# Performance work log

Measured on AMD Instinct MI355X. Metric: run time of the kernel, lower is better.

## Reference

```python
import jax, jax.numpy as jnp
import numpy as np

B, L, S, D = 32, 256, 4, 512
H = L * S  # history_capacity
TGB = 128
VOCAB = 50000
LN_EPS = 1e-5


def _layer_norm(x, gamma, beta):
    mu = jnp.mean(x, axis=-1, keepdims=True)
    var = jnp.var(x, axis=-1, keepdims=True)
    return (x - mu) * jax.lax.rsqrt(var + LN_EPS) * gamma + beta


def setup_inputs() -> dict:
    key = jax.random.key(0)
    ks = jax.random.split(key, 16)
    inp = {
        'embed_table': jax.random.normal(ks[0], (VOCAB, D), jnp.float32) * 0.02,
        'time_gap_emb': jax.random.normal(ks[1], (TGB + 1, D), jnp.float32) * 0.02,
        'seq_id_emb': jax.random.normal(ks[2], (S + 1, D), jnp.float32) * 0.02,
        'pos_emb': jax.random.normal(ks[3], (L, D), jnp.float32) * 0.02,
        'ln_gamma': jnp.ones((5 * D,), jnp.float32),
        'ln_beta': jnp.zeros((5 * D,), jnp.float32),
        'w1': jax.random.normal(ks[4], (5 * D, 4 * D), jnp.float32) * (1.0 / np.sqrt(5 * D)),
        'b1': jnp.zeros((4 * D,), jnp.float32),
        'w2': jax.random.normal(ks[5], (4 * D, D), jnp.float32) * (1.0 / np.sqrt(4 * D)),
        'b2': jnp.zeros((D,), jnp.float32),
        'empty_tokens': jax.random.normal(ks[6], (S, D), jnp.float32) * 0.02,
        'history_tokens': jax.random.randint(ks[7], (B, H), 0, VOCAB, jnp.int64 if jax.config.jax_enable_x64 else jnp.int32),
        'post_tokens': jax.random.randint(ks[8], (B, H), 0, VOCAB),
        'author_tokens': jax.random.randint(ks[9], (B, H), 0, VOCAB),
        'action_tokens': jax.random.randint(ks[10], (B, H), 0, VOCAB),
        'time_gap': jax.random.randint(ks[11], (B, H), 0, TGB + 1),
        'group_ids': jax.random.randint(ks[12], (B, H), 0, S + 1),
        'lengths': jax.random.randint(ks[13], (B,), 0, H + 1),
    }
    return inp


def reference(embed_table, time_gap_emb, seq_id_emb, pos_emb, ln_gamma, ln_beta,
              w1, b1, w2, b2, empty_tokens,
              history_tokens, post_tokens, author_tokens, action_tokens,
              time_gap, group_ids, lengths):
    # padded-dense validity mask: positions < lengths  [B,H]
    history_mask = jnp.arange(H)[None, :] < lengths[:, None]
    # zero out padded tokens (to_padded_dense pads with 0)
    hm_i = history_mask.astype(history_tokens.dtype)
    ht = history_tokens * hm_i
    pt = post_tokens * hm_i
    at = author_tokens * hm_i
    ct = action_tokens * hm_i
    tg = jnp.clip(time_gap * hm_i, 0, TGB)
    gid = group_ids * hm_i

    # event feature: 4 token embeds + time-gap embed -> [B,H,5D]
    event_inputs = jnp.concatenate(
        [embed_table[ht], embed_table[pt], embed_table[at], embed_table[ct],
         time_gap_emb[tg]], axis=-1)
    x = _layer_norm(event_inputs, ln_gamma, ln_beta)
    h = jax.nn.silu(x @ w1 + b1)          # dropout is eval-mode no-op
    event_tokens = h @ w2 + b2            # [B,H,D]

    # per-(batch, group) bucketization: keep last L valid positions of each group
    grp = jnp.arange(1, S + 1)
    mask_bs = history_mask[:, None, :] & (gid[:, None, :] == grp[None, :, None])  # [B,S,H]
    cum = jnp.cumsum(mask_bs.astype(jnp.int32), axis=-1)
    count = cum[..., -1]                                  # [B,S]
    offset = jnp.maximum(count - L, 0)                    # drop all but last L
    rank0 = cum - 1
    keep = mask_bs & (rank0 >= offset[..., None])
    dest = jnp.where(keep, rank0 - offset[..., None], L)  # slot L = dump slot

    def scatter_one(tokens, d):  # tokens [H,D], d [H] -> [L,D]
        return jnp.zeros((L + 1, D), tokens.dtype).at[d].set(tokens)[:L]

    # vmap over batch then group
    states = jax.vmap(lambda tok, ds: jax.vmap(lambda d: scatter_one(tok, d))(ds))(
        event_tokens, dest)                               # [B,S,L,D]

    # empty groups get the learned empty token at slot 0
    is_empty = (count == 0)                               # [B,S]
    slot0 = (jnp.arange(L) == 0)                          # [L]
    states = jnp.where((is_empty[:, :, None] & slot0[None, None, :])[..., None],
                       empty_tokens[None, :, None, :], states)
    kept = jnp.where(is_empty, 1, jnp.minimum(count, L))  # [B,S]
    sequence_mask = jnp.arange(L)[None, None, :] < kept[..., None]  # [B,S,L]

    states = states + pos_emb[None, None, :, :] + seq_id_emb[1:][None, :, None, :]
    states = states * sequence_mask[..., None].astype(states.dtype)
    return states, sequence_mask
```

## Files before the change

### kernel.cpp

```cpp
#include <hip/hip_runtime.h>
#include <hip/hip_bf16.h>
#include <stdint.h>

#define NB 32
#define NL 256
#define NS 4
#define ND 512
#define NH 1024
#define FIVE_D 2560
#define HID 2048
#define MMAX 32768

typedef __bf16 bf16_t;
typedef __bf16 bf16x4 __attribute__((ext_vector_type(4)));
typedef __bf16 bf16x8 __attribute__((ext_vector_type(8)));
typedef float f32x4 __attribute__((ext_vector_type(4)));

__device__ __forceinline__ void async_ld16(const void* g, void* l) {
  __builtin_amdgcn_global_load_lds(
      (__attribute__((address_space(1))) void*)(uintptr_t)g,
      (__attribute__((address_space(3))) void*)(uintptr_t)l, 16, 0, 0);
}

__global__ void build_index_kernel(const int* __restrict__ group_ids,
                                   const int* __restrict__ lengths,
                                   int* __restrict__ n_rows,
                                   int* __restrict__ row_src,
                                   int* __restrict__ row_dst,
                                   const float* __restrict__ empty_tokens,
                                   const float* __restrict__ pos_emb,
                                   const float* __restrict__ seq_emb,
                                   float* __restrict__ out,
                                   float* __restrict__ mask) {
  const int g = blockIdx.x >> 2;
  const int qtr = blockIdx.x & 3;
  const int b = g >> 2, s = g & 3;
  const int t = threadIdx.x;
  const int lane = t & 63, w = t >> 6;
  int len = lengths[b];
  len = len < 0 ? 0 : (len > NH ? NH : len);
  const int* gi = group_ids + b * NH;

  __shared__ int wtot[16];
  __shared__ int sbase;

  bool valid[4];
#pragma unroll
  for (int c = 0; c < 4; ++c) {
    int h = c * 256 + t;
    valid[c] = (h < len) && (gi[h] == s + 1);
    unsigned long long m = __ballot(valid[c]);
    if (lane == 0) wtot[c * 4 + w] = __popcll(m);
  }
  __syncthreads();

  int pre[16];
  int run = 0;
#pragma unroll
  for (int i = 0; i < 16; ++i) { pre[i] = run; run += wtot[i]; }
  const int count = run;
  const int keff = count < NL ? count : NL;
  const int offset = count - keff;

  const bool empty = (count == 0);
  const int start = empty ? 1 : keff;

  if (qtr == 0) {
    if (t == 0) sbase = atomicAdd(n_rows, keff);
    __syncthreads();
    const int base = sbase;

    const unsigned long long lt = (1ull << lane) - 1ull;
#pragma unroll
    for (int c = 0; c < 4; ++c) {
      unsigned long long m = __ballot(valid[c]);
      if (valid[c]) {
        int rank = pre[c * 4 + w] + __popcll(m & lt);
        if (rank >= offset) {
          int slot = rank - offset;
          row_src[base + slot] = b * NH + c * 256 + t;
          row_dst[base + slot] = g * NL + slot;
        }
      }
    }

    const int keptm = empty ? 1 : keff;
    mask[g * NL + t] = (t < keptm) ? 1.f : 0.f;

    if (empty) {
      float* basep = out + (size_t)g * NL * ND;
      for (int d = t; d < ND; d += 256)
        basep[d] = empty_tokens[s * ND + d] + pos_emb[d] +
                   seq_emb[(s + 1) * ND + d];
    }
  }

  int lo = qtr * 64; if (lo < start) lo = start;
  const int hi = qtr * 64 + 64;
  if (lo < hi) {
    uint4* p = (uint4*)(out + (size_t)g * NL * ND);
    uint4 z; z.x = z.y = z.z = z.w = 0u;
    for (int i = lo * (ND / 4) + t; i < hi * (ND / 4); i += 256) p[i] = z;
  }
}

template <int KD, int NDIM>
__global__ void transpose_cvt_kernel(const float* __restrict__ src,
                                     bf16_t* __restrict__ dst) {
  __shared__ float tile[32][33];
  int k0 = blockIdx.y * 32, n0 = blockIdx.x * 32;
  int tx = threadIdx.x & 31, ty = threadIdx.x >> 5;
#pragma unroll
  for (int i = 0; i < 32; i += 8)
    tile[ty + i][tx] = src[(size_t)(k0 + ty + i) * NDIM + n0 + tx];
  __syncthreads();
#pragma unroll
  for (int i = 0; i < 32; i += 8)
    dst[(size_t)(n0 + ty + i) * KD + k0 + tx] = (bf16_t)tile[tx][ty + i];
}

__launch_bounds__(256)
__global__ void gather_ln_kernel(const float* __restrict__ embed,
                                 const float* __restrict__ tg_emb,
                                 const int* __restrict__ ht,
                                 const int* __restrict__ pt,
                                 const int* __restrict__ at,
                                 const int* __restrict__ ct,
                                 const int* __restrict__ tg,
                                 const float* __restrict__ gamma,
                                 const float* __restrict__ beta,
                                 const int* __restrict__ n_rows,
                                 const int* __restrict__ row_src,
                                 int row_base, int chunk,
                                 bf16_t* __restrict__ X) {
  const int l = threadIdx.x & 63;
  const int wid = blockIdx.x * 4 + (threadIdx.x >> 6);
  const int wstride = gridDim.x * 4;
  const int M = *n_rows;
  int lim = row_base + chunk;
  if (lim > M) lim = M;

  const int o = l * 4;

  for (int r = row_base + wid; r < lim; r += wstride) {
    const int rl = r - row_base;
    const int pos = row_src[r];

    const float* s0 = embed + (size_t)ht[pos] * ND;
    const float* s1 = embed + (size_t)pt[pos] * ND;
    const float* s2 = embed + (size_t)at[pos] * ND;
    const float* s3 = embed + (size_t)ct[pos] * ND;
    int tgv = tg[pos];
    tgv = tgv < 0 ? 0 : (tgv > 128 ? 128 : tgv);
    const float* s4 = tg_emb + (size_t)tgv * ND;

    float4 v0 = *(const float4*)(s0 + o);
    float4 v1 = *(const float4*)(s0 + 256 + o);
    float4 v2 = *(const float4*)(s1 + o);
    float4 v3 = *(const float4*)(s1 + 256 + o);
    float4 v4 = *(const float4*)(s2 + o);
    float4 v5 = *(const float4*)(s2 + 256 + o);
    float4 v6 = *(const float4*)(s3 + o);
    float4 v7 = *(const float4*)(s3 + 256 + o);
    float4 v8 = *(const float4*)(s4 + o);
    float4 v9 = *(const float4*)(s4 + 256 + o);

    float sum = 0.f, sq = 0.f;
#define ACC(vk)                                                              \
    do {                                                                     \
      sum += vk.x + vk.y + vk.z + vk.w;                                      \
      sq += vk.x * vk.x + vk.y * vk.y + vk.z * vk.z + vk.w * vk.w;           \
    } while (0)
    ACC(v0); ACC(v1); ACC(v2); ACC(v3); ACC(v4);
    ACC(v5); ACC(v6); ACC(v7); ACC(v8); ACC(v9);
#undef ACC
#pragma unroll
    for (int off = 32; off > 0; off >>= 1) {
      sum += __shfl_xor(sum, off);
      sq += __shfl_xor(sq, off);
    }
    const float mu = sum * (1.f / FIVE_D);
    const float var = sq * (1.f / FIVE_D) - mu * mu;
    const float rstd = rsqrtf(var + 1e-5f);

    bf16_t* xr = X + (size_t)rl * FIVE_D;
#define LN_STORE(vk, kofs)                                                   \
    do {                                                                     \
      float4 gm = *(const float4*)(gamma + (kofs) + o);                      \
      float4 bt = *(const float4*)(beta + (kofs) + o);                       \
      bf16x4 ov;                                                             \
      ov[0] = (bf16_t)((vk.x - mu) * rstd * gm.x + bt.x);                    \
      ov[1] = (bf16_t)((vk.y - mu) * rstd * gm.y + bt.y);                    \
      ov[2] = (bf16_t)((vk.z - mu) * rstd * gm.z + bt.z);                    \
      ov[3] = (bf16_t)((vk.w - mu) * rstd * gm.w + bt.w);                    \
      *(bf16x4*)(xr + (kofs) + o) = ov;                                      \
    } while (0)
    LN_STORE(v0, 0);    LN_STORE(v1, 256);
    LN_STORE(v2, 512);  LN_STORE(v3, 768);
    LN_STORE(v4, 1024); LN_STORE(v5, 1280);
    LN_STORE(v6, 1536); LN_STORE(v7, 1792);
    LN_STORE(v8, 2048); LN_STORE(v9, 2304);
#undef LN_STORE
  }
}

#define FENCE asm volatile("" ::: "memory")
#define BARRIER do { FENCE; __builtin_amdgcn_s_barrier(); FENCE; } while (0)
#define WAIT_VM(n) asm volatile("s_waitcnt vmcnt(" #n ")" ::: "memory")

template <int KD, int LDC>
__launch_bounds__(512, 2)
__global__ void gemm256p4_kernel(const bf16_t* __restrict__ A,
                                 const bf16_t* __restrict__ Bt,
                                 const int* __restrict__ nrows_p,
                                 int row_base,
                                 const float* __restrict__ bias,
                                 bf16_t* __restrict__ Cb) {
  static_assert(KD % 64 == 0 && KD / 64 >= 2, "KD");
  const int M = *nrows_p;
  const int m0 = blockIdx.x * 256;
  if (row_base + m0 >= M) return;
  const int n0 = blockIdx.y * 256;

  extern __shared__ char smem[];

  const int t = threadIdx.x;
  const int lane = t & 63;
  const int wv = t >> 6;
  const int wm = wv >> 2;
  const int wn = wv & 3;
  const int l15 = lane & 15;
  const int l4 = lane >> 4;

  const int r0 = t >> 3;
  const int sq = (t & 7) ^ (r0 & 7);
  const bf16_t* Ab = A + (size_t)(m0 + r0) * KD + sq * 8;
  const bf16_t* Bb =
      Bt + (size_t)(n0 + (r0 >> 5) * 64 + (r0 & 31)) * KD + sq * 8;
  const int dst16 = t * 16;

  const int cs0 = (l4 ^ (l15 & 7)) << 4;
  const int cs1 = cs0 ^ 64;
  const int arow = (wm * 64 + l15) * 128;
  const int brow = (wn * 32 + l15) * 128;

  f32x4 acc[2][2][4][2] = {};
  bf16x8 a[4][2], bl[2][2], bh[2][2];

#define SA(dbuf, h, kofs)                                                    \
  do {                                                                       \
    char* _d = smem + (dbuf) * 65536 + (h) * 16384 + dst16;                  \
    async_ld16(Ab + (size_t)((h) * 64) * KD + (kofs), _d);                   \
    async_ld16(Ab + (size_t)((h) * 64 + 128) * KD + (kofs), _d + 8192);      \
  } while (0)
#define SB(dbuf, h, kofs)                                                    \
  do {                                                                       \
    char* _d = smem + (dbuf) * 65536 + 32768 + (h) * 16384 + dst16;          \
    async_ld16(Bb + (size_t)((h) * 32) * KD + (kofs), _d);                   \
    async_ld16(Bb + (size_t)((h) * 32 + 128) * KD + (kofs), _d + 8192);      \
  } while (0)
#define LA(cbuf, ih)                                                         \
  do {                                                                       \
    const char* _s = smem + (cbuf) * 65536 + (ih) * 16384 + arow;            \
    _Pragma("unroll") for (int _i = 0; _i < 4; ++_i) {                       \
      a[_i][0] = *(const bf16x8*)(_s + _i * 2048 + cs0);                     \
      a[_i][1] = *(const bf16x8*)(_s + _i * 2048 + cs1);                     \
    }                                                                        \
  } while (0)
#define LB(dst, cbuf, jh)                                                    \
  do {                                                                       \
    const char* _s = smem + (cbuf) * 65536 + 32768 + (jh) * 16384 + brow;    \
    _Pragma("unroll") for (int _j = 0; _j < 2; ++_j) {                       \
      dst[_j][0] = *(const bf16x8*)(_s + _j * 2048 + cs0);                   \
      dst[_j][1] = *(const bf16x8*)(_s + _j * 2048 + cs1);                   \
    }                                                                        \
  } while (0)
#define MMA(ih, jh, B)                                                       \
  do {                                                                       \
    _Pragma("unroll") for (int _i = 0; _i < 4; ++_i)                         \
    _Pragma("unroll") for (int _j = 0; _j < 2; ++_j) {                       \
      acc[ih][jh][_i][_j] = __builtin_amdgcn_mfma_f32_16x16x32_bf16(         \
          a[_i][0], B[_j][0], acc[ih][jh][_i][_j], 0, 0, 0);                 \
      acc[ih][jh][_i][_j] = __builtin_amdgcn_mfma_f32_16x16x32_bf16(         \
          a[_i][1], B[_j][1], acc[ih][jh][_i][_j], 0, 0, 0);                 \
    }                                                                        \
  } while (0)

  constexpr int NT = KD / 64;

  SA(0, 0, 0);
  SB(0, 0, 0);
  SB(0, 1, 0);
  SA(0, 1, 0);

  int c = 0;
  for (int tk = 1; tk < NT; ++tk) {
    const int kn = tk * 64;
    const int d = c ^ 1;
    WAIT_VM(4);
    BARRIER;
    LA(c, 0);
    LB(bl, c, 0);
    SA(d, 0, kn);
    __builtin_amdgcn_s_setprio(1);
    MMA(0, 0, bl);
    __builtin_amdgcn_s_setprio(0);
    WAIT_VM(4);
    BARRIER;
    LB(bh, c, 1);
    SB(d, 0, kn);
    __builtin_amdgcn_s_setprio(1);
    MMA(0, 1, bh);
    __builtin_amdgcn_s_setprio(0);
    WAIT_VM(4);
    BARRIER;
    LA(c, 1);
    SB(d, 1, kn);
    __builtin_amdgcn_s_setprio(1);
    MMA(1, 1, bh);
    __builtin_amdgcn_s_setprio(0);
    SA(d, 1, kn);
    __builtin_amdgcn_s_setprio(1);
    MMA(1, 0, bl);
    __builtin_amdgcn_s_setprio(0);
    BARRIER;
    c = d;
  }

  WAIT_VM(4);
  BARRIER;
  LA(c, 0);
  LB(bl, c, 0);
  MMA(0, 0, bl);
  WAIT_VM(2);
  BARRIER;
  LB(bh, c, 1);
  MMA(0, 1, bh);
  WAIT_VM(0);
  BARRIER;
  LA(c, 1);
  MMA(1, 1, bh);
  MMA(1, 0, bl);

#pragma unroll
  for (int ih = 0; ih < 2; ++ih)
#pragma unroll
    for (int i = 0; i < 4; ++i) {
      const int rbase = m0 + wm * 128 + ih * 64 + i * 16 + l4 * 4;
#pragma unroll
      for (int jh = 0; jh < 2; ++jh)
#pragma unroll
        for (int j = 0; j < 2; ++j) {
          const int n = n0 + wn * 64 + jh * 32 + j * 16 + l15;
          const float bn = bias[n];
#pragma unroll
          for (int q = 0; q < 4; ++q) {
            float v = acc[ih][jh][i][j][q] + bn;
            v = v / (1.f + __expf(-v));
            Cb[(size_t)(rbase + q) * LDC + n] = (bf16_t)v;
          }
        }
    }
#undef SA
#undef SB
#undef LA
#undef LB
#undef MMA
}

template <int KD>
__launch_bounds__(512, 4)
__global__ void gemm128_scatter_kernel(const bf16_t* __restrict__ A,
                                       const bf16_t* __restrict__ Bt,
                                       const int* __restrict__ nrows_p,
                                       int row_base,
                                       const float* __restrict__ bias,
                                       const int* __restrict__ row_dst,
                                       const float* __restrict__ pos_emb,
                                       const float* __restrict__ seq_emb,
                                       float* __restrict__ out) {
  static_assert(KD % 64 == 0 && KD / 64 >= 2, "KD");
  const int M = *nrows_p;
  const int m0 = blockIdx.x * 128;
  if (row_base + m0 >= M) return;
  const int n0 = blockIdx.y * 128;

  extern __shared__ char smem[];

  const int t = threadIdx.x;
  const int lane = t & 63;
  const int wv = t >> 6;
  const int wm = wv >> 1;
  const int wn = wv & 1;
  const int l15 = lane & 15;
  const int l4 = lane >> 4;

  const int r0 = t >> 3;
  const int sq = (t & 7) ^ (r0 & 7);
  const bf16_t* Ab = A + (size_t)(m0 + r0) * KD + sq * 8;
  const bf16_t* Bb = Bt + (size_t)(n0 + r0) * KD + sq * 8;
  const int dst16 = t * 16;

  const int cs0 = (l4 ^ (l15 & 7)) << 4;
  const int cs1 = cs0 ^ 64;
  const int arow = (wm * 32 + l15) * 128;
  const int brow = (wn * 64 + l15) * 128;

  f32x4 acc[2][4] = {};
  bf16x8 a[2][2], b[4][2];

#define STAGE_A2(dbuf, kofs)                                                 \
  do {                                                                       \
    char* _d = smem + (dbuf) * 32768 + dst16;                                \
    async_ld16(Ab + (kofs), _d);                                             \
    async_ld16(Ab + (size_t)64 * KD + (kofs), _d + 8192);                    \
  } while (0)
#define STAGE_B2(dbuf, kofs)                                                 \
  do {                                                                       \
    char* _d = smem + (dbuf) * 32768 + 16384 + dst16;                        \
    async_ld16(Bb + (kofs), _d);                                             \
    async_ld16(Bb + (size_t)64 * KD + (kofs), _d + 8192);                    \
  } while (0)
#define LOAD_A2(cbuf)                                                        \
  do {                                                                       \
    const char* _s = smem + (cbuf) * 32768 + arow;                           \
    _Pragma("unroll") for (int _i = 0; _i < 2; ++_i) {                       \
      a[_i][0] = *(const bf16x8*)(_s + _i * 2048 + cs0);                     \
      a[_i][1] = *(const bf16x8*)(_s + _i * 2048 + cs1);                     \
    }                                                                        \
  } while (0)
#define LOAD_B2(cbuf)                                                        \
  do {                                                                       \
    const char* _s = smem + (cbuf) * 32768 + 16384 + brow;                   \
    _Pragma("unroll") for (int _j = 0; _j < 4; ++_j) {                       \
      b[_j][0] = *(const bf16x8*)(_s + _j * 2048 + cs0);                     \
      b[_j][1] = *(const bf16x8*)(_s + _j * 2048 + cs1);                     \
    }                                                                        \
  } while (0)
#define MMA2                                                                 \
  do {                                                                       \
    _Pragma("unroll") for (int _i = 0; _i < 2; ++_i)                         \
    _Pragma("unroll") for (int _j = 0; _j < 4; ++_j) {                       \
      acc[_i][_j] = __builtin_amdgcn_mfma_f32_16x16x32_bf16(                 \
          a[_i][0], b[_j][0], acc[_i][_j], 0, 0, 0);                         \
      acc[_i][_j] = __builtin_amdgcn_mfma_f32_16x16x32_bf16(                 \
          a[_i][1], b[_j][1], acc[_i][_j], 0, 0, 0);                         \
    }                                                                        \
  } while (0)

  constexpr int NT = KD / 64;

  STAGE_A2(0, 0);
  STAGE_B2(0, 0);

  int c = 0;
  for (int tk = 1; tk < NT; ++tk) {
    const int kn = tk * 64;
    const int d = c ^ 1;
    STAGE_A2(d, kn);
    WAIT_VM(2);
    BARRIER;
    LOAD_A2(c);
    LOAD_B2(c);
    STAGE_B2(d, kn);
    __builtin_amdgcn_s_setprio(1);
    MMA2;
    __builtin_amdgcn_s_setprio(0);
    BARRIER;
    c = d;
  }

  WAIT_VM(0);
  BARRIER;
  LOAD_A2(c);
  LOAD_B2(c);
  MMA2;

#pragma unroll
  for (int i = 0; i < 2; ++i) {
    int mbase = m0 + wm * 32 + i * 16 + l4 * 4;
#pragma unroll
    for (int q = 0; q < 4; ++q) {
      int r = mbase + q;
      if (row_base + r >= M) continue;
      int dst = row_dst[row_base + r];
      int slot = dst & (NL - 1);
      int sg = (dst >> 8) & 3;
#pragma unroll
      for (int j = 0; j < 4; ++j) {
        int n = n0 + wn * 64 + j * 16 + l15;
        float v = acc[i][j][q] + bias[n] + pos_emb[slot * ND + n] +
                  seq_emb[(sg + 1) * ND + n];
        out[(size_t)dst * ND + n] = v;
      }
    }
  }
#undef STAGE_A2
#undef STAGE_B2
#undef LOAD_A2
#undef LOAD_B2
#undef MMA2
}

extern "C" void kernel_launch(void* const* d_in, const int* in_sizes, int n_in,
                              void* d_out, int out_size, void* d_ws,
                              size_t ws_size, hipStream_t stream) {
  const float* embed_table = (const float*)d_in[0];
  const float* time_gap_emb = (const float*)d_in[1];
  const float* seq_id_emb = (const float*)d_in[2];
  const float* pos_emb = (const float*)d_in[3];
  const float* ln_gamma = (const float*)d_in[4];
  const float* ln_beta = (const float*)d_in[5];
  const float* w1 = (const float*)d_in[6];
  const float* b1 = (const float*)d_in[7];
  const float* w2 = (const float*)d_in[8];
  const float* b2 = (const float*)d_in[9];
  const float* empty_tokens = (const float*)d_in[10];
  const int* history_tokens = (const int*)d_in[11];
  const int* post_tokens = (const int*)d_in[12];
  const int* author_tokens = (const int*)d_in[13];
  const int* action_tokens = (const int*)d_in[14];
  const int* time_gap = (const int*)d_in[15];
  const int* group_ids = (const int*)d_in[16];
  const int* lengths = (const int*)d_in[17];

  const size_t fixed = 266240 + (size_t)(HID * FIVE_D + ND * HID) * 2;
  int chunk, nchunk;
  if (ws_size >= fixed + (size_t)32768 * 9216) { chunk = 32768; nchunk = 1; }
  else if (ws_size >= fixed + (size_t)16384 * 9216) { chunk = 16384; nchunk = 2; }
  else { chunk = 8192; nchunk = 4; }

  char* ws = (char*)d_ws;
  int* n_rows = (int*)ws;
  int* row_src = (int*)(ws + 4096);
  int* row_dst = (int*)(ws + 4096 + 131072);
  bf16_t* W1T = (bf16_t*)(ws + 266240);
  bf16_t* W2T = W1T + (size_t)HID * FIVE_D;
  bf16_t* Xc = W2T + (size_t)ND * HID;
  bf16_t* H1c = Xc + (size_t)chunk * FIVE_D;

  float* out_states = (float*)d_out;
  float* out_mask = out_states + (size_t)NB * NS * NL * ND;

  (void)hipFuncSetAttribute(
      reinterpret_cast<const void*>(gemm256p4_kernel<FIVE_D, HID>),
      hipFuncAttributeMaxDynamicSharedMemorySize, 131072);
  (void)hipFuncSetAttribute(
      reinterpret_cast<const void*>(gemm128_scatter_kernel<HID>),
      hipFuncAttributeMaxDynamicSharedMemorySize, 65536);

  hipMemsetAsync(n_rows, 0, 4, stream);

  build_index_kernel<<<NB * NS * 4, 256, 0, stream>>>(
      group_ids, lengths, n_rows, row_src, row_dst, empty_tokens, pos_emb,
      seq_id_emb, out_states, out_mask);

  transpose_cvt_kernel<FIVE_D, HID>
      <<<dim3(HID / 32, FIVE_D / 32), 256, 0, stream>>>(w1, W1T);
  transpose_cvt_kernel<HID, ND>
      <<<dim3(ND / 32, HID / 32), 256, 0, stream>>>(w2, W2T);

  for (int c = 0; c < nchunk; ++c) {
    int row_base = c * chunk;
    gather_ln_kernel<<<2048, 256, 0, stream>>>(
        embed_table, time_gap_emb, history_tokens, post_tokens, author_tokens,
        action_tokens, time_gap, ln_gamma, ln_beta, n_rows, row_src, row_base,
        chunk, Xc);

    gemm256p4_kernel<FIVE_D, HID>
        <<<dim3(chunk / 256, HID / 256), 512, 131072, stream>>>(
            Xc, W1T, n_rows, row_base, b1, H1c);

    gemm128_scatter_kernel<HID>
        <<<dim3(chunk / 128, ND / 128), 512, 65536, stream>>>(
            H1c, W2T, n_rows, row_base, b2, row_dst, pos_emb, seq_id_emb,
            out_states);
  }
}
```

Measured before the change: 392.6 us.

## Double-buffer A fragments in registers and prefetch next tile before barrier

Restructures the GEMM main loop so the A fragments for both M halves live in separate register sets (aA/aB). The first A/B fragments of the next K tile are read from LDS at the end of each iteration. Global-to-LDS async loads are regrouped so that each barrier phase issues two halves. The aim is to cut barrier stalls and LDS-read latency exposed before the MFMA chains. The cost is extra VGPR pressure, which could reduce occupancy or cause spills.

After: 403.6 us. +2.8%, slower.

```diff
diff --git a/kernel.cpp b/kernel.cpp
--- a/kernel.cpp
+++ b/kernel.cpp
@@ -245,7 +245,7 @@
   const int brow = (wn * 32 + l15) * 128;
 
   f32x4 acc[2][2][4][2] = {};
-  bf16x8 a[4][2], bl[2][2], bh[2][2];
+  bf16x8 aA[4][2], aB[4][2], bl[2][2], bh[2][2];
 
 #define SA(dbuf, h, kofs)                                                    \
   do {                                                                       \
@@ -259,12 +259,12 @@
     async_ld16(Bb + (size_t)((h) * 32) * KD + (kofs), _d);                   \
     async_ld16(Bb + (size_t)((h) * 32 + 128) * KD + (kofs), _d + 8192);      \
   } while (0)
-#define LA(cbuf, ih)                                                         \
+#define LA(dst, cbuf, ih)                                                    \
   do {                                                                       \
     const char* _s = smem + (cbuf) * 65536 + (ih) * 16384 + arow;            \
     _Pragma("unroll") for (int _i = 0; _i < 4; ++_i) {                       \
-      a[_i][0] = *(const bf16x8*)(_s + _i * 2048 + cs0);                     \
-      a[_i][1] = *(const bf16x8*)(_s + _i * 2048 + cs1);                     \
+      dst[_i][0] = *(const bf16x8*)(_s + _i * 2048 + cs0);                   \
+      dst[_i][1] = *(const bf16x8*)(_s + _i * 2048 + cs1);                   \
     }                                                                        \
   } while (0)
 #define LB(dst, cbuf, jh)                                                    \
@@ -275,14 +275,14 @@
       dst[_j][1] = *(const bf16x8*)(_s + _j * 2048 + cs1);                   \
     }                                                                        \
   } while (0)
-#define MMA(ih, jh, B)                                                       \
+#define MMA(ih, jh, Am, Bm)                                                  \
   do {                                                                       \
     _Pragma("unroll") for (int _i = 0; _i < 4; ++_i)                         \
     _Pragma("unroll") for (int _j = 0; _j < 2; ++_j) {                       \
       acc[ih][jh][_i][_j] = __builtin_amdgcn_mfma_f32_16x16x32_bf16(         \
-          a[_i][0], B[_j][0], acc[ih][jh][_i][_j], 0, 0, 0);                 \
+          Am[_i][0], Bm[_j][0], acc[ih][jh][_i][_j], 0, 0, 0);               \
       acc[ih][jh][_i][_j] = __builtin_amdgcn_mfma_f32_16x16x32_bf16(         \
-          a[_i][1], B[_j][1], acc[ih][jh][_i][_j], 0, 0, 0);                 \
+          Am[_i][1], Bm[_j][1], acc[ih][jh][_i][_j], 0, 0, 0);               \
     }                                                                        \
   } while (0)
 
@@ -292,55 +292,52 @@
   SB(0, 0, 0);
   SB(0, 1, 0);
   SA(0, 1, 0);
+  WAIT_VM(2);
+  BARRIER;
+  LA(aA, 0, 0);
+  LB(bl, 0, 0);
 
   int c = 0;
   for (int tk = 1; tk < NT; ++tk) {
     const int kn = tk * 64;
     const int d = c ^ 1;
-    WAIT_VM(4);
-    BARRIER;
-    LA(c, 0);
-    LB(bl, c, 0);
+    LB(bh, c, 1);
     SA(d, 0, kn);
+    SB(d, 0, kn);
     __builtin_amdgcn_s_setprio(1);
-    MMA(0, 0, bl);
+    MMA(0, 0, aA, bl);
     __builtin_amdgcn_s_setprio(0);
     WAIT_VM(4);
     BARRIER;
-    LB(bh, c, 1);
-    SB(d, 0, kn);
+    LA(aB, c, 1);
+    SB(d, 1, kn);
+    SA(d, 1, kn);
     __builtin_amdgcn_s_setprio(1);
-    MMA(0, 1, bh);
+    MMA(0, 1, aA, bh);
+    __builtin_amdgcn_s_setprio(0);
+    __builtin_amdgcn_s_setprio(1);
+    MMA(1, 1, aB, bh);
     __builtin_amdgcn_s_setprio(0);
     WAIT_VM(4);
     BARRIER;
-    LA(c, 1);
-    SB(d, 1, kn);
     __builtin_amdgcn_s_setprio(1);
-    MMA(1, 1, bh);
+    MMA(1, 0, aB, bl);
     __builtin_amdgcn_s_setprio(0);
-    SA(d, 1, kn);
-    __builtin_amdgcn_s_setprio(1);
-    MMA(1, 0, bl);
-    __builtin_amdgcn_s_setprio(0);
+    LA(aA, d, 0);
+    LB(bl, d, 0);
+    WAIT_VM(2);
     BARRIER;
     c = d;
   }
 
-  WAIT_VM(4);
-  BARRIER;
-  LA(c, 0);
-  LB(bl, c, 0);
-  MMA(0, 0, bl);
-  WAIT_VM(2);
-  BARRIER;
   LB(bh, c, 1);
-  MMA(0, 1, bh);
+  MMA(0, 0, aA, bl);
   WAIT_VM(0);
   BARRIER;
-  LA(c, 1);
-  MMA(1, 1, bh);
-  MMA(1, 0, bl);
+  LA(aB, c, 1);
+  MMA(0, 1, aA, bh);
+  MMA(1, 1, aB, bh);
+  MMA(1, 0, aB, bl);
 
 #pragma unroll
   for (int ih = 0; ih < 2; ++ih)
```
